# Kernel tuning notes

Measured on AMD Instinct MI355X. Metric: run time of the kernel, lower is better.

## Reference

```python
import jax, jax.numpy as jnp
import numpy as np

N_ENT = 50000   # entities (nodes)
N_REL = 500     # relations
DEG = 32        # regular in-degree of the full KG
TOPK = 10       # topk in-edges kept per node by dgl.sampling.select_topk
H_DIM = 256
N_HEADS = 4
HEAD_DIM = H_DIM // N_HEADS
NEG_SLOPE = 0.2


def _leaky(x):
    return jnp.where(x >= 0, x, NEG_SLOPE * x)


def setup_inputs() -> dict:
    key = jax.random.key(0)
    ks = jax.random.split(key, 8)
    s = 0.05
    return {
        'ent_emb': jax.random.normal(ks[0], (N_ENT, H_DIM), dtype=jnp.float32),
        'rel_emb': jax.random.normal(ks[1], (N_REL, H_DIM), dtype=jnp.float32),
        'W': jax.random.normal(ks[2], (N_HEADS, H_DIM, HEAD_DIM), dtype=jnp.float32) * s,
        'W_r': jax.random.normal(ks[3], (N_HEADS, H_DIM, HEAD_DIM), dtype=jnp.float32) * s,
        'a': jax.random.normal(ks[4], (N_HEADS, 3 * HEAD_DIM), dtype=jnp.float32) * s,
        'neigh_w': jax.random.normal(ks[5], (H_DIM, H_DIM), dtype=jnp.float32) * s,
        'src': jax.random.randint(ks[6], (N_ENT, DEG), 0, N_ENT),   # src node of each in-edge of node n
        'rel_id': jax.random.randint(ks[7], (N_ENT, DEG), 0, N_REL),
    }


def reference(ent_emb, rel_emb, W, W_r, a, neigh_w, src, rel_id):
    # ---- head-0 scores used for top-k in-edge sampling (select_topk, edge_dir='in') ----
    emb_t0 = ent_emb @ W[0]          # [N, hd]
    rel_t0 = rel_emb @ W_r[0]        # [R, hd]
    a0 = a[0]
    # concat([src,dst,rel]) @ a  ==  src@a_src + dst@a_dst + rel@a_rel
    s_src = emb_t0 @ a0[:HEAD_DIM]                 # [N]
    s_dst = emb_t0 @ a0[HEAD_DIM:2 * HEAD_DIM]     # [N]
    s_rel = rel_t0 @ a0[2 * HEAD_DIM:]             # [R]
    score0 = _leaky(s_src[src] + s_dst[:, None] + s_rel[rel_id])   # [N, DEG]
    _, top_idx = jax.lax.top_k(score0, TOPK)                        # [N, K]
    src_sel = jnp.take_along_axis(src, top_idx, axis=1)             # [N, K]
    rel_sel = jnp.take_along_axis(rel_id, top_idx, axis=1)          # [N, K]

    # ---- all heads on the sampled subgraph (vectorized over heads) ----
    emb_t = jnp.einsum('nd,hde->hne', ent_emb, W)     # [H, N, hd]
    rel_t = jnp.einsum('rd,hde->hre', rel_emb, W_r)   # [H, R, hd]
    a3 = a.reshape(N_HEADS, 3, HEAD_DIM)
    ss = jnp.einsum('hne,he->hn', emb_t, a3[:, 0])    # [H, N]
    sd = jnp.einsum('hne,he->hn', emb_t, a3[:, 1])    # [H, N]
    sr = jnp.einsum('hre,he->hr', rel_t, a3[:, 2])    # [H, R]
    scores = _leaky(ss[:, src_sel] + sd[:, :, None] + sr[:, rel_sel])  # [H, N, K]
    norm = jax.nn.softmax(scores, axis=-1)            # edge-softmax over in-edges per dst

    # comp_op == 'add' : u_add_e, weighted by attention, summed into dst
    comp = emb_t[:, src_sel] + rel_t[:, rel_sel]      # [H, N, K, hd]
    neigh = jnp.einsum('hnke,hnk->hne', comp, norm)   # [H, N, hd]

    neigh = jnp.transpose(neigh, (1, 0, 2)).reshape(ent_emb.shape[0], H_DIM)  # concat heads
    return jnp.tanh(neigh @ neigh_w)                  # bn disabled (cfg.bn=False)
```

## Files before the change

### kernel.cpp

```cpp
#include <hip/hip_runtime.h>
#include <math.h>

#define N_ENT 50000
#define N_REL 500
#define DEG 32
#define TOPK 10
#define H_DIM 256
#define N_HEADS 4
#define HEAD_DIM 64

typedef __attribute__((ext_vector_type(8))) short short8v;
typedef __attribute__((ext_vector_type(4))) float f32x4;

constexpr size_t OFF_SSRC0 = 0;
constexpr size_t OFF_SR0   = 400000;
constexpr size_t OFF_U0    = 404000;
constexpr size_t OFF_V0    = 406048;
constexpr size_t OFF_SS    = 408096;
constexpr size_t OFF_SSR   = 2008096;
constexpr size_t OFF_U8    = 2024096;
constexpr size_t OFF_V8    = 2032288;
constexpr size_t OFF_B1H   = 2040480;
constexpr size_t OFF_B2H   = 2302624;
constexpr size_t OFF_B3H   = 2564768;
constexpr size_t OFF_RPK   = 2826912;
constexpr size_t OFF_EAH   = 3089056;
constexpr size_t OFF_EMBBF = 28713632;
constexpr size_t OFF_RELBF = 54313632;
constexpr size_t WS_NEED   = 54569632;

__device__ __forceinline__ float leaky(float x) { return x >= 0.f ? x : 0.2f * x; }

__device__ __forceinline__ unsigned short bf16_rne(float x) {
    unsigned int u = __float_as_uint(x);
    unsigned int r = u + 0x7fffu + ((u >> 16) & 1u);
    return (unsigned short)(r >> 16);
}
__device__ __forceinline__ float bf2f(unsigned short x) {
    return __uint_as_float((unsigned)x << 16);
}

__device__ __forceinline__ size_t pack_off(int row, int d) {
    return ((size_t)(row >> 4) * 8 + (d >> 5)) * 512 +
           (((d >> 3) & 3) * 16 + (row & 15)) * 8 + (d & 7);
}

__global__ __launch_bounds__(256) void setup_kernel(
    const float* __restrict__ W, const float* __restrict__ W_r,
    const float* __restrict__ a, const float* __restrict__ nw,
    float* __restrict__ U8, double* __restrict__ u0,
    float* __restrict__ V8, double* __restrict__ v0,
    unsigned short* __restrict__ b1h, unsigned short* __restrict__ b2h,
    unsigned short* __restrict__ b3h)
{
    const int bid = blockIdx.x;
    const int tid = threadIdx.x;
    if (bid == 0) {
        int d = tid;
        #pragma unroll
        for (int h = 0; h < N_HEADS; ++h) {
            float ss = 0.f, sd = 0.f;
            #pragma unroll
            for (int e = 0; e < HEAD_DIM; ++e) {
                float w = W[h * 16384 + d * 64 + e];
                ss += w * a[h * 192 + e];
                sd += w * a[h * 192 + 64 + e];
            }
            U8[d * 8 + h] = ss;
            U8[d * 8 + 4 + h] = sd;
        }
        double s0 = 0.0;
        #pragma unroll
        for (int e = 0; e < HEAD_DIM; ++e)
            s0 += (double)W[d * 64 + e] * (double)a[e];
        u0[d] = s0;
    } else if (bid == 1) {
        int d = tid;
        #pragma unroll
        for (int h = 0; h < N_HEADS; ++h) {
            float sv = 0.f;
            #pragma unroll
            for (int e = 0; e < HEAD_DIM; ++e)
                sv += W_r[h * 16384 + d * 64 + e] * a[h * 192 + 128 + e];
            V8[d * 8 + h] = sv;
            V8[d * 8 + 4 + h] = 0.f;
        }
        double s0 = 0.0;
        #pragma unroll
        for (int e = 0; e < HEAD_DIM; ++e)
            s0 += (double)W_r[d * 64 + e] * (double)a[128 + e];
        v0[d] = s0;
    } else {
        int n = bid - 2;
        int k = tid;
        int h = n >> 6, e = n & 63;
        float x1 = W[h * 16384 + k * 64 + e];
        float x2 = nw[k * 256 + n];
        float x3 = W_r[h * 16384 + k * 64 + e];
        size_t off = pack_off(n, k);
        b1h[off] = bf16_rne(x1);
        b2h[off] = bf16_rne(x2);
        b3h[off] = bf16_rne(x3);
    }
}

__global__ __launch_bounds__(256) void ss_kernel(
    const float* __restrict__ ent, const float* __restrict__ relm,
    const float* __restrict__ U8, const double* __restrict__ u0,
    const float* __restrict__ V8, const double* __restrict__ v0,
    float* __restrict__ SS, double* __restrict__ ssrc0, unsigned short* __restrict__ apk,
    float* __restrict__ SSR, double* __restrict__ sr0, unsigned short* __restrict__ rpk)
{
    const int tid = threadIdx.x;
    const int l = tid & 63;
    const int el = l & 31;
    const int q2 = l >> 5;

    const bool isent = blockIdx.x < 2048;
    const float* X = isent ? ent : relm;
    const float* U8v = isent ? U8 : V8;
    const double* u0v = isent ? u0 : v0;
    float* SSout = isent ? SS : SSR;
    double* s0out = isent ? ssrc0 : sr0;
    unsigned short* Xpk = isent ? apk : rpk;
    const int N = isent ? N_ENT : N_REL;
    const int wave0 = isent ? ((blockIdx.x * 256 + tid) >> 6)
                            : (((blockIdx.x - 2048) * 256 + tid) >> 6);
    const int nwaves = isent ? 8192 : 252;

    float uu[8][8];
    #pragma unroll
    for (int i = 0; i < 8; ++i) {
        float4 a4 = *(const float4*)(U8v + (el * 8 + i) * 8);
        float4 b4 = *(const float4*)(U8v + (el * 8 + i) * 8 + 4);
        uu[i][0] = a4.x; uu[i][1] = a4.y; uu[i][2] = a4.z; uu[i][3] = a4.w;
        uu[i][4] = b4.x; uu[i][5] = b4.y; uu[i][6] = b4.z; uu[i][7] = b4.w;
    }
    double ud[8];
    #pragma unroll
    for (int i = 0; i < 8; ++i) ud[i] = u0v[el * 8 + i];

    const int jout = ((el & 1) << 2) | (el & 2) | ((el >> 2) & 1);
    const int half = N / 2;

    int p = wave0;
    float4 x1, x2;
    if (p < half) {
        int n0 = p * 2 + q2;
        x1 = *(const float4*)(X + (size_t)n0 * 256 + el * 8);
        x2 = *(const float4*)(X + (size_t)n0 * 256 + el * 8 + 4);
    }
    for (; p < half; p += nwaves) {
        const int n = p * 2 + q2;
        const float4 cx1 = x1, cx2 = x2;
        const int np = p + nwaves;
        if (np < half) {
            int n1 = np * 2 + q2;
            x1 = *(const float4*)(X + (size_t)n1 * 256 + el * 8);
            x2 = *(const float4*)(X + (size_t)n1 * 256 + el * 8 + 4);
        }
        float xs[8] = {cx1.x, cx1.y, cx1.z, cx1.w, cx2.x, cx2.y, cx2.z, cx2.w};

        short8v ov;
        #pragma unroll
        for (int i = 0; i < 8; ++i) ov[i] = (short)bf16_rne(xs[i]);
        *(short8v*)(Xpk + pack_off(n, el * 8)) = ov;

        float pj[8] = {0.f, 0.f, 0.f, 0.f, 0.f, 0.f, 0.f, 0.f};
        double pd = 0.0;
        #pragma unroll
        for (int i = 0; i < 8; ++i) {
            #pragma unroll
            for (int j = 0; j < 8; ++j) pj[j] += xs[i] * uu[i][j];
            pd += (double)xs[i] * ud[i];
        }

        const bool b1 = (el & 1);
        float q[4];
        #pragma unroll
        for (int j = 0; j < 4; ++j) {
            float mine = b1 ? pj[j + 4] : pj[j];
            float send = b1 ? pj[j] : pj[j + 4];
            q[j] = mine + __shfl_xor(send, 1);
        }
        const bool b2 = (el & 2);
        float r2[2];
        #pragma unroll
        for (int j = 0; j < 2; ++j) {
            float mine = b2 ? q[j + 2] : q[j];
            float send = b2 ? q[j] : q[j + 2];
            r2[j] = mine + __shfl_xor(send, 2);
        }
        const bool b4 = (el & 4);
        {
            float mine = b4 ? r2[1] : r2[0];
            float send = b4 ? r2[0] : r2[1];
            r2[0] = mine + __shfl_xor(send, 4);
        }
        r2[0] += __shfl_xor(r2[0], 8);
        r2[0] += __shfl_xor(r2[0], 16);

        #pragma unroll
        for (int off = 1; off < 32; off <<= 1) pd += __shfl_xor(pd, off);

        if (el < 8) SSout[(size_t)n * 8 + jout] = r2[0];
        if (el == 0) s0out[n] = pd;
    }
}

__global__ __launch_bounds__(256, 4) void gemm_hi(
    const unsigned short* __restrict__ A1, const unsigned short* __restrict__ B1,
    unsigned short* __restrict__ C1, int M1, int nb1,
    const unsigned short* __restrict__ A2, const unsigned short* __restrict__ B2,
    unsigned short* __restrict__ C2, int M2)
{
    const int tid = threadIdx.x;
    const int l = tid & 63;
    const int w = tid >> 6;
    const int rl = l & 15;
    const int ql = l >> 4;

    const int b = blockIdx.x;
    const unsigned short* Apk = (b < nb1) ? A1 : A2;
    const unsigned short* Bh  = (b < nb1) ? B1 : B2;
    unsigned short* C         = (b < nb1) ? C1 : C2;
    const int M               = (b < nb1) ? M1 : M2;
    const int bm              = ((b < nb1) ? b : (b - nb1)) * 64;

    const unsigned short* ab = Apk + (size_t)(bm >> 4) * 4096 + l * 8;
    const unsigned short* bhb = Bh + (size_t)w * 16384 + l * 8;

    f32x4 acc[4][4];
    #pragma unroll
    for (int i = 0; i < 4; ++i)
        #pragma unroll
        for (int j = 0; j < 4; ++j) acc[i][j] = (f32x4){0.f, 0.f, 0.f, 0.f};

    #pragma unroll
    for (int ks = 0; ks < 8; ++ks) {
        short8v ah[4], bh[4];
        #pragma unroll
        for (int mf = 0; mf < 4; ++mf)
            ah[mf] = *(const short8v*)(ab + mf * 4096 + ks * 512);
        #pragma unroll
        for (int nf = 0; nf < 4; ++nf)
            bh[nf] = *(const short8v*)(bhb + nf * 4096 + ks * 512);
        #pragma unroll
        for (int mf = 0; mf < 4; ++mf)
            #pragma unroll
            for (int nf = 0; nf < 4; ++nf)
                acc[mf][nf] = __builtin_amdgcn_mfma_f32_16x16x32_bf16(ah[mf], bh[nf], acc[mf][nf], 0, 0, 0);
    }

    #pragma unroll
    for (int mf = 0; mf < 4; ++mf) {
        int row0 = bm + mf * 16 + ql * 4;
        #pragma unroll
        for (int nf = 0; nf < 4; ++nf) {
            int c = w * 64 + nf * 16 + rl;
            #pragma unroll
            for (int j = 0; j < 4; ++j) {
                int r = row0 + j;
                if (r < M)
                    C[(size_t)r * 256 + c] = bf16_rne(acc[mf][nf][j]);
            }
        }
    }
}

__global__ __launch_bounds__(256, 3) void node_kernel(
    const int* __restrict__ src, const int* __restrict__ relid,
    const float* __restrict__ SS, const double* __restrict__ ssrc0,
    const float* __restrict__ SSR, const double* __restrict__ sr0,
    const unsigned short* __restrict__ emb_bf, const unsigned short* __restrict__ rel_bf,
    unsigned short* __restrict__ napk)
{
    __shared__ float wls[8][32][4];

    const int tid = threadIdx.x;
    const int l = tid & 63;
    const int el = l & 31;
    const int hb = l & 32;
    const int nib = tid >> 5;
    const int n = blockIdx.x * 8 + nib;

    const int sd_ = src[n * DEG + el];
    const int rd_ = relid[n * DEG + el];
    const double sc0 = ssrc0[sd_] + sr0[rd_];

    int cnt = 0;
    #pragma unroll
    for (int j = 0; j < DEG; ++j) {
        double sj = __shfl(sc0, hb | j);
        cnt += (sj > sc0 || (sj == sc0 && j < el)) ? 1 : 0;
    }
    const bool sel = (cnt < TOPK);
    const unsigned mask = (unsigned)(__ballot(sel) >> hb);

    float scx = -1e30f, scy = -1e30f, scz = -1e30f, scw = -1e30f;
    if (sel) {
        float4 ssv = *(const float4*)(SS + (size_t)sd_ * 8);
        float4 srv = *(const float4*)(SSR + (size_t)rd_ * 8);
        float4 sdv = *(const float4*)(SS + (size_t)n * 8 + 4);
        scx = leaky(ssv.x + sdv.x + srv.x);
        scy = leaky(ssv.y + sdv.y + srv.y);
        scz = leaky(ssv.z + sdv.z + srv.z);
        scw = leaky(ssv.w + sdv.w + srv.w);
    }

    float mx = scx, my = scy, mz = scz, mw = scw;
    #pragma unroll
    for (int off = 1; off < 32; off <<= 1) {
        mx = fmaxf(mx, __shfl_xor(mx, off));
        my = fmaxf(my, __shfl_xor(my, off));
        mz = fmaxf(mz, __shfl_xor(mz, off));
        mw = fmaxf(mw, __shfl_xor(mw, off));
    }
    float ex = sel ? __expf(scx - mx) : 0.f;
    float ey = sel ? __expf(scy - my) : 0.f;
    float ez = sel ? __expf(scz - mz) : 0.f;
    float ew = sel ? __expf(scw - mw) : 0.f;
    float sx = ex, sy = ey, sz = ez, sw = ew;
    #pragma unroll
    for (int off = 1; off < 32; off <<= 1) {
        sx += __shfl_xor(sx, off);
        sy += __shfl_xor(sy, off);
        sz += __shfl_xor(sz, off);
        sw += __shfl_xor(sw, off);
    }

    if (sel) {
        float4 wv; wv.x = ex; wv.y = ey; wv.z = ez; wv.w = ew;
        *(float4*)&wls[nib][el][0] = wv;
    }

    const int h = el >> 3;
    const float sh = h == 0 ? sx : h == 1 ? sy : h == 2 ? sz : sw;
    const float rsh = 1.f / sh;

    int lks[TOPK], sk[TOPK], rk[TOPK];
    unsigned mm = mask;
    #pragma unroll
    for (int k = 0; k < TOPK; ++k) {
        lks[k] = __builtin_ctz(mm);
        mm &= mm - 1;
        sk[k] = __shfl(sd_, hb | lks[k]);
        rk[k] = __shfl(rd_, hb | lks[k]);
    }

    short8v ev[TOPK], rv[TOPK];
    #pragma unroll
    for (int k = 0; k < TOPK; ++k)
        ev[k] = *(const short8v*)(emb_bf + (size_t)sk[k] * 256 + el * 8);
    #pragma unroll
    for (int k = 0; k < TOPK; ++k)
        rv[k] = *(const short8v*)(rel_bf + (size_t)rk[k] * 256 + el * 8);
    asm volatile("s_waitcnt vmcnt(0)" ::: "memory");

    float acc[8] = {0.f, 0.f, 0.f, 0.f, 0.f, 0.f, 0.f, 0.f};
    #pragma unroll
    for (int k = 0; k < TOPK; ++k) {
        float w = wls[nib][lks[k]][h] * rsh;
        #pragma unroll
        for (int j = 0; j < 8; ++j)
            acc[j] += w * (bf2f((unsigned short)ev[k][j]) + bf2f((unsigned short)rv[k][j]));
    }

    short8v ov;
    #pragma unroll
    for (int j = 0; j < 8; ++j) ov[j] = (short)bf16_rne(acc[j]);
    *(short8v*)(napk + pack_off(n, el * 8)) = ov;
}

__global__ __launch_bounds__(256, 4) void gemm_out(
    const unsigned short* __restrict__ Apk, const unsigned short* __restrict__ Bpkh,
    float* __restrict__ Cout, int M)
{
    const int tid = threadIdx.x;
    const int l = tid & 63;
    const int w = tid >> 6;
    const int bm = blockIdx.x * 64;
    const int rl = l & 15;
    const int ql = l >> 4;

    const unsigned short* ab = Apk + (size_t)(bm >> 4) * 4096 + l * 8;
    const unsigned short* bhb = Bpkh + (size_t)w * 16384 + l * 8;

    f32x4 acc[4][4];
    #pragma unroll
    for (int i = 0; i < 4; ++i)
        #pragma unroll
        for (int j = 0; j < 4; ++j) acc[i][j] = (f32x4){0.f, 0.f, 0.f, 0.f};

    #pragma unroll
    for (int ks = 0; ks < 8; ++ks) {
        short8v ah[4], bh[4];
        #pragma unroll
        for (int mf = 0; mf < 4; ++mf)
            ah[mf] = *(const short8v*)(ab + mf * 4096 + ks * 512);
        #pragma unroll
        for (int nf = 0; nf < 4; ++nf)
            bh[nf] = *(const short8v*)(bhb + nf * 4096 + ks * 512);
        #pragma unroll
        for (int mf = 0; mf < 4; ++mf)
            #pragma unroll
            for (int nf = 0; nf < 4; ++nf)
                acc[mf][nf] = __builtin_amdgcn_mfma_f32_16x16x32_bf16(ah[mf], bh[nf], acc[mf][nf], 0, 0, 0);
    }

    #pragma unroll
    for (int mf = 0; mf < 4; ++mf) {
        int row0 = bm + mf * 16 + ql * 4;
        #pragma unroll
        for (int nf = 0; nf < 4; ++nf) {
            int c = w * 64 + nf * 16 + rl;
            #pragma unroll
            for (int j = 0; j < 4; ++j) {
                int r = row0 + j;
                if (r < M) {
                    float v = acc[mf][nf][j];
                    Cout[(size_t)r * 256 + c] = 1.f - 2.f / (__expf(2.f * v) + 1.f);
                }
            }
        }
    }
}

extern "C" void kernel_launch(void* const* d_in, const int* in_sizes, int n_in,
                              void* d_out, int out_size, void* d_ws, size_t ws_size,
                              hipStream_t stream) {
    const float* ent  = (const float*)d_in[0];
    const float* rel  = (const float*)d_in[1];
    const float* W    = (const float*)d_in[2];
    const float* W_r  = (const float*)d_in[3];
    const float* a    = (const float*)d_in[4];
    const float* nw   = (const float*)d_in[5];
    const int*   srcp = (const int*)d_in[6];
    const int*   ridp = (const int*)d_in[7];
    float* out = (float*)d_out;

    if (ws_size < WS_NEED) return;

    char* ws = (char*)d_ws;
    double* ssrc0 = (double*)(ws + OFF_SSRC0);
    double* sr0   = (double*)(ws + OFF_SR0);
    double* u0    = (double*)(ws + OFF_U0);
    double* v0    = (double*)(ws + OFF_V0);
    float*  SS    = (float*)(ws + OFF_SS);
    float*  SSR   = (float*)(ws + OFF_SSR);
    float*  U8    = (float*)(ws + OFF_U8);
    float*  V8    = (float*)(ws + OFF_V8);
    unsigned short* b1h = (unsigned short*)(ws + OFF_B1H);
    unsigned short* b2h = (unsigned short*)(ws + OFF_B2H);
    unsigned short* b3h = (unsigned short*)(ws + OFF_B3H);
    unsigned short* rpk = (unsigned short*)(ws + OFF_RPK);
    unsigned short* apk = (unsigned short*)(ws + OFF_EAH);
    unsigned short* embbf = (unsigned short*)(ws + OFF_EMBBF);
    unsigned short* relbf = (unsigned short*)(ws + OFF_RELBF);
    unsigned short* napk = apk;

    setup_kernel<<<258, 256, 0, stream>>>(W, W_r, a, nw, U8, u0, V8, v0,
                                          b1h, b2h, b3h);
    ss_kernel<<<2111, 256, 0, stream>>>(ent, rel, U8, u0, V8, v0,
                                        SS, ssrc0, apk, SSR, sr0, rpk);
    gemm_hi<<<790, 256, 0, stream>>>(apk, b1h, embbf, N_ENT, 782,
                                     rpk, b3h, relbf, N_REL);
    node_kernel<<<6250, 256, 0, stream>>>(srcp, ridp, SS, ssrc0, SSR, sr0,
                                          embbf, relbf, napk);
    gemm_out<<<782, 256, 0, stream>>>(napk, b2h, out, N_ENT);
}
```

Before: 146.9 us.

## Replace cross-lane shuffles in node kernel with LDS broadcast and compaction

The top-k ranking loop now reads the 32 candidate scores from shared memory instead of 32 double-precision shuffles. Selected edge ids and weights are compacted into shared slots, so the ctz/shuffle loop that gathered neighbour indices goes away. The softmax max-reduction is dropped, and the four per-head sum reductions are merged with a transpose-style butterfly. Skipping the max subtraction relies on attention scores staying small enough that exp does not overflow. Packing ids into 16 bits relies on entity and relation counts staying below 65536.

```diff
diff --git a/kernel.cpp b/kernel.cpp
--- a/kernel.cpp
+++ b/kernel.cpp
@@ -275,7 +275,10 @@
     const unsigned short* __restrict__ emb_bf, const unsigned short* __restrict__ rel_bf,
     unsigned short* __restrict__ napk)
 {
-    __shared__ float wls[8][32][4];
+    __shared__ double scs[8][33];
+    __shared__ unsigned idsS[8][12];
+    __shared__ float wtsS[8][10][4];
+    __shared__ float sumsS[8][4];
 
     const int tid = threadIdx.x;
     const int l = tid & 63;
@@ -287,80 +290,75 @@
     const int sd_ = src[n * DEG + el];
     const int rd_ = relid[n * DEG + el];
     const double sc0 = ssrc0[sd_] + sr0[rd_];
+    scs[nib][el] = sc0;
 
     int cnt = 0;
     #pragma unroll
     for (int j = 0; j < DEG; ++j) {
-        double sj = __shfl(sc0, hb | j);
+        double sj = scs[nib][j];
         cnt += (sj > sc0 || (sj == sc0 && j < el)) ? 1 : 0;
     }
     const bool sel = (cnt < TOPK);
     const unsigned mask = (unsigned)(__ballot(sel) >> hb);
-
-    float scx = -1e30f, scy = -1e30f, scz = -1e30f, scw = -1e30f;
+    const int pos = __popc(mask & ((1u << el) - 1u));
+
+    float ex = 0.f, ey = 0.f, ez = 0.f, ew = 0.f;
     if (sel) {
         float4 ssv = *(const float4*)(SS + (size_t)sd_ * 8);
         float4 srv = *(const float4*)(SSR + (size_t)rd_ * 8);
         float4 sdv = *(const float4*)(SS + (size_t)n * 8 + 4);
-        scx = leaky(ssv.x + sdv.x + srv.x);
-        scy = leaky(ssv.y + sdv.y + srv.y);
-        scz = leaky(ssv.z + sdv.z + srv.z);
-        scw = leaky(ssv.w + sdv.w + srv.w);
-    }
-
-    float mx = scx, my = scy, mz = scz, mw = scw;
-    #pragma unroll
-    for (int off = 1; off < 32; off <<= 1) {
-        mx = fmaxf(mx, __shfl_xor(mx, off));
-        my = fmaxf(my, __shfl_xor(my, off));
-        mz = fmaxf(mz, __shfl_xor(mz, off));
-        mw = fmaxf(mw, __shfl_xor(mw, off));
-    }
-    float ex = sel ? __expf(scx - mx) : 0.f;
-    float ey = sel ? __expf(scy - my) : 0.f;
-    float ez = sel ? __expf(scz - mz) : 0.f;
-    float ew = sel ? __expf(scw - mw) : 0.f;
-    float sx = ex, sy = ey, sz = ez, sw = ew;
-    #pragma unroll
-    for (int off = 1; off < 32; off <<= 1) {
-        sx += __shfl_xor(sx, off);
-        sy += __shfl_xor(sy, off);
-        sz += __shfl_xor(sz, off);
-        sw += __shfl_xor(sw, off);
-    }
-
-    if (sel) {
+        ex = __expf(leaky(ssv.x + sdv.x + srv.x));
+        ey = __expf(leaky(ssv.y + sdv.y + srv.y));
+        ez = __expf(leaky(ssv.z + sdv.z + srv.z));
+        ew = __expf(leaky(ssv.w + sdv.w + srv.w));
+        idsS[nib][pos] = (unsigned)sd_ | ((unsigned)rd_ << 16);
         float4 wv; wv.x = ex; wv.y = ey; wv.z = ez; wv.w = ew;
-        *(float4*)&wls[nib][el][0] = wv;
-    }
+        *(float4*)&wtsS[nib][pos][0] = wv;
+    }
+
+    float p0, p1;
+    {
+        const bool b1 = (el & 1);
+        float m0 = b1 ? ez : ex, s0 = b1 ? ex : ez;
+        float m1 = b1 ? ew : ey, s1 = b1 ? ey : ew;
+        p0 = m0 + __shfl_xor(s0, 1);
+        p1 = m1 + __shfl_xor(s1, 1);
+    }
+    float qsum;
+    {
+        const bool b2 = (el & 2);
+        float m = b2 ? p1 : p0, s = b2 ? p0 : p1;
+        qsum = m + __shfl_xor(s, 2);
+    }
+    qsum += __shfl_xor(qsum, 4);
+    qsum += __shfl_xor(qsum, 8);
+    qsum += __shfl_xor(qsum, 16);
+    if (el < 4) sumsS[nib][((el & 1) << 1) | ((el >> 1) & 1)] = qsum;
 
     const int h = el >> 3;
-    const float sh = h == 0 ? sx : h == 1 ? sy : h == 2 ? sz : sw;
-    const float rsh = 1.f / sh;
-
-    int lks[TOPK], sk[TOPK], rk[TOPK];
-    unsigned mm = mask;
+
+    int skA[TOPK], rkA[TOPK];
     #pragma unroll
     for (int k = 0; k < TOPK; ++k) {
-        lks[k] = __builtin_ctz(mm);
-        mm &= mm - 1;
-        sk[k] = __shfl(sd_, hb | lks[k]);
-        rk[k] = __shfl(rd_, hb | lks[k]);
+        unsigned idk = idsS[nib][k];
+        skA[k] = (int)(idk & 0xFFFFu);
+        rkA[k] = (int)(idk >> 16);
     }
 
     short8v ev[TOPK], rv[TOPK];
     #pragma unroll
     for (int k = 0; k < TOPK; ++k)
-        ev[k] = *(const short8v*)(emb_bf + (size_t)sk[k] * 256 + el * 8);
+        ev[k] = *(const short8v*)(emb_bf + (size_t)skA[k] * 256 + el * 8);
     #pragma unroll
     for (int k = 0; k < TOPK; ++k)
-        rv[k] = *(const short8v*)(rel_bf + (size_t)rk[k] * 256 + el * 8);
+        rv[k] = *(const short8v*)(rel_bf + (size_t)rkA[k] * 256 + el * 8);
     asm volatile("s_waitcnt vmcnt(0)" ::: "memory");
 
+    const float rsh = 1.f / sumsS[nib][h];
     float acc[8] = {0.f, 0.f, 0.f, 0.f, 0.f, 0.f, 0.f, 0.f};
     #pragma unroll
     for (int k = 0; k < TOPK; ++k) {
-        float w = wls[nib][lks[k]][h] * rsh;
+        float w = wtsS[nib][k][h] * rsh;
         #pragma unroll
         for (int j = 0; j < 8; ++j)
             acc[j] += w * (bf2f((unsigned short)ev[k][j]) + bf2f((unsigned short)rv[k][j]));
```

Result: no change. 146.3 us (-0.4%).
